# Kernel tuning notes

Hardware: AMD Instinct MI355X
Metric: run time of the kernel (lower is better)

Reference implementation:

```python
import jax, jax.numpy as jnp
import numpy as np

D_HEAD = 128


def setup_inputs() -> dict:
    key = jax.random.key(0)
    k1, k2, k3 = jax.random.split(key, 3)
    batch, num_q, seq_len, d = 16, 64, 4096, D_HEAD
    query = jax.random.normal(k1, (batch, num_q, d), dtype=jnp.float32)
    keys = jax.random.normal(k2, (batch, seq_len, d), dtype=jnp.float32)
    values = jax.random.normal(k3, (batch, seq_len, d), dtype=jnp.float32)
    return {"query": query, "keys": keys, "values": values}


def reference(query, keys, values):
    # AttentionJacobian.forward with 3D query -> compute_attention_jacobian_batched
    # J[b,q] = scale * ( sum_n a[b,q,n] v[b,n] k[b,n]^T  -  (a V)[b,q] ((a K)[b,q])^T )
    d_k = keys.shape[-1]
    scale = d_k ** (-0.5)
    scores = jnp.einsum('bqd,bnd->bqn', query, keys) * scale
    attn_weights = jax.nn.softmax(scores, axis=-1)            # (b, q, n)
    attn_outputs = jnp.einsum('bqn,bnv->bqv', attn_weights, values)
    # term1 without materializing (b, q, n, v, k): fuse as single contraction
    term1 = jnp.einsum('bqn,bnv,bnk->bqvk', attn_weights, values, keys)
    weighted_keys_sum = jnp.einsum('bqn,bnk->bqk', attn_weights, keys)
    term2 = jnp.einsum('bqv,bqk->bqvk', attn_outputs, weighted_keys_sum)
    jacobians = scale * (term1 - term2)                       # (b, q, d_v, d_k)
    return jacobians
```

## Files before the change

### kernel.cpp

```cpp
#include <hip/hip_runtime.h>
#include <stdint.h>

typedef _Float16 f16;
typedef _Float16 half8 __attribute__((ext_vector_type(8)));
typedef float f32x4 __attribute__((ext_vector_type(4)));

#define BATCH 16
#define NQ 64
#define SL 4096
#define DH 128


typedef __attribute__((address_space(3))) uint8_t lds8_t;
typedef __attribute__((address_space(1))) uint8_t glb8_t;

__device__ __forceinline__ void gload16(const void* g, void* l) {
  __builtin_amdgcn_global_load_lds((const glb8_t*)g, (lds8_t*)l, 16, 0, 0);
}

__global__ __launch_bounds__(256) void kprep(const float* __restrict__ Kg,
                                             const float* __restrict__ Vg,
                                             f16* __restrict__ Kt,
                                             f16* __restrict__ Vt) {
  __shared__ f16 Ld[128][130];
  const int blk = blockIdx.x;
  const int b = blk >> 6;
  const int tensor = (blk >> 5) & 1;
  const int chunk = blk & 31;
  const float* src = tensor ? Vg : Kg;
  f16* dst = tensor ? Vt : Kt;
  const int t = threadIdx.x;
  const int n0 = chunk * 128;
  {
    const int d = t & 127;
    const int nl = t >> 7;
    const float* s = src + ((size_t)b * SL + n0 + nl) * DH + d;
    for (int it = 0; it < 64; ++it)
      Ld[d][nl + it * 2] = (f16)s[(size_t)it * 2 * DH];
  }
  __syncthreads();
  {
    const int r = t & 15;
    const int kc = (t >> 4) & 3;
    const int w = t >> 6;
    char* dstb = (char*)(dst + (size_t)b * DH * SL);
#pragma unroll
    for (int tl = 0; tl < 4; ++tl)
#pragma unroll
      for (int hh = 0; hh < 2; ++hh) {
        const int dhi = w + hh * 4;
        const int d = dhi * 16 + r;
        const int nl = tl * 32 + kc * 8;
        const half8 v = *(const half8*)&Ld[d][nl];
        *(half8*)(dstb + (size_t)(chunk * 4 + tl) * 8192 + dhi * 1024 +
                  kc * 256 + r * 16) = v;
      }
  }
}

__global__ __launch_bounds__(256) void kscore(const float* __restrict__ Q,
                                              const f16* __restrict__ Kt,
                                              f16* __restrict__ E) {
  const int blk = (blockIdx.x & 7) * 64 + (blockIdx.x >> 3);
  __shared__ float Qs[8][128];
  const int b = blk >> 5;
  const int qg = (blk >> 2) & 7;
  const int ns = blk & 3;
  const int t = threadIdx.x;
  for (int i = t; i < 8 * 128; i += 256)
    Qs[i >> 7][i & 127] = Q[((size_t)b * NQ + qg * 8 + (i >> 7)) * DH + (i & 127)];
  __syncthreads();
  const int w = t >> 6, l = t & 63;
  const int q0 = (w >> 1) * 4;
  const int nbase = ns * 1024 + (w & 1) * 512 + l * 8;
  const f16* kb = Kt + (size_t)b * DH * SL + (size_t)(nbase >> 5) * 4096 +
                  (size_t)((nbase >> 3) & 3) * 128;
  float acc[4][8] = {};
  for (int d = 0; d < DH; ++d) {
    const half8 kv = *(const half8*)(kb + (d >> 4) * 512 + (d & 15) * 8);
    float kf[8];
#pragma unroll
    for (int j = 0; j < 8; ++j) kf[j] = (float)kv[j];
#pragma unroll
    for (int qi = 0; qi < 4; ++qi) {
      const float qv = Qs[q0 + qi][d];
#pragma unroll
      for (int j = 0; j < 8; ++j) acc[qi][j] += qv * kf[j];
    }
  }
  const float scl = 0.08838834764831845f;
#pragma unroll
  for (int qi = 0; qi < 4; ++qi) {
    half8 ev;
#pragma unroll
    for (int j = 0; j < 8; ++j) ev[j] = (f16)__expf(acc[qi][j] * scl);
    *(half8*)&E[((size_t)b * NQ + qg * 8 + q0 + qi) * SL + nbase] = ev;
  }
}

__global__ __launch_bounds__(256) void kreduce(const f16* __restrict__ E,
                                               float* __restrict__ denom) {
  const int gw = blockIdx.x * 4 + (threadIdx.x >> 6);
  const int lane = threadIdx.x & 63;
  const f16* e = E + (size_t)gw * SL;
  float s = 0.f;
#pragma unroll
  for (int i = 0; i < 8; ++i) {
    const half8 h = *(const half8*)(e + i * 512 + lane * 8);
#pragma unroll
    for (int j = 0; j < 8; ++j) s += (float)h[j];
  }
  for (int off = 1; off < 64; off <<= 1) s += __shfl_xor(s, off);
  if (lane == 0) denom[gw] = s;
}

__global__ __launch_bounds__(256) void kev(const f16* __restrict__ Vt,
                                           const f16* __restrict__ Kt,
                                           const f16* __restrict__ E,
                                           float* __restrict__ EVp,
                                           float* __restrict__ EKp) {
  const int blk = (blockIdx.x & 7) * 32 + (blockIdx.x >> 3);
  const int b = blk >> 4;
  const int tensor = (blk >> 3) & 1;
  const int qq = (blk >> 1) & 3;
  const int nh = blk & 1;
  const char* src = (const char*)((tensor ? Kt : Vt) + (size_t)b * DH * SL);
  float* dst = (tensor ? EKp : EVp) +
               ((size_t)nh * BATCH * NQ + (size_t)b * NQ + qq * 16) * DH;
  const f16* Eb = E + ((size_t)b * NQ + qq * 16) * SL;
  const int t = threadIdx.x, w = t >> 6, l = t & 63;
  f32x4 acc[2] = {};
  for (int n0 = nh * 2048; n0 < nh * 2048 + 2048; n0 += 32) {
    const half8 a0 =
        *(const half8*)(src + (size_t)(n0 >> 5) * 8192 + w * 1024 + l * 16);
    const half8 a1 =
        *(const half8*)(src + (size_t)(n0 >> 5) * 8192 + (w + 4) * 1024 + l * 16);
    const half8 b0 =
        *(const half8*)(Eb + (size_t)(l & 15) * SL + n0 + (l >> 4) * 8);
    acc[0] = __builtin_amdgcn_mfma_f32_16x16x32_f16(a0, b0, acc[0], 0, 0, 0);
    acc[1] = __builtin_amdgcn_mfma_f32_16x16x32_f16(a1, b0, acc[1], 0, 0, 0);
  }
#pragma unroll
  for (int sv2 = 0; sv2 < 2; ++sv2) {
    const int q = l & 15;
    const int row = (w + sv2 * 4) * 16 + (l >> 4) * 4;
    *(f32x4*)&dst[(size_t)q * DH + row] = acc[sv2];
  }
}

__global__ __launch_bounds__(256, 2) void kjac(
    const f16* __restrict__ Vt, const f16* __restrict__ Kt,
    const f16* __restrict__ E, const float* __restrict__ EV,
    const float* __restrict__ EK, const float* __restrict__ denom,
    float* __restrict__ out) {
  __shared__ __align__(16) f16 Vl[4][4096];
  __shared__ __align__(16) f16 Kl[4][4096];

  const int blk = (blockIdx.x & 7) * 64 + (blockIdx.x >> 3);
  const int b = blk >> 5;
  const int q0 = (blk & 31) * 2;
  const int t = threadIdx.x, w = t >> 6, l = t & 63;
  const int sA = (w >> 1) * 4;
  const int sB = (w & 1) * 4;
  const char* vtb = (const char*)(Vt + (size_t)b * DH * SL);
  const char* ktb = (const char*)(Kt + (size_t)b * DH * SL);
  const f16* Eb = E + ((size_t)b * NQ + q0) * SL;

  f32x4 acc[2][4][4] = {};
  half8 eA[2], eB[2];

#define STAGE(tile)                                                          \
  {                                                                          \
    const int bf = (tile) & 3;                                               \
    const size_t gb = (size_t)(tile) * 8192 + t * 16;                        \
    gload16(vtb + gb, (char*)Vl[bf] + t * 16);                               \
    gload16(vtb + gb + 4096, (char*)Vl[bf] + t * 16 + 4096);                 \
    gload16(ktb + gb, (char*)Kl[bf] + t * 16);                               \
    gload16(ktb + gb + 4096, (char*)Kl[bf] + t * 16 + 4096);                 \
  }

#define ELOAD(dst, tile)                                                     \
  {                                                                          \
    const int nn = (tile) * 32 + (l >> 4) * 8;                               \
    dst[0] = *(const half8*)(Eb + nn);                                       \
    dst[1] = *(const half8*)(Eb + SL + nn);                                  \
  }

#define COMPUTE(tile, e)                                                     \
  {                                                                          \
    const f16* vbuf = Vl[(tile) & 3];                                        \
    const f16* kbuf = Kl[(tile) & 3];                                        \
    half8 vf[4], kf[4];                                                      \
    _Pragma("unroll") for (int i = 0; i < 4; ++i) vf[i] =                    \
        *(const half8*)(vbuf + (sA + i) * 512 + l * 8);                      \
    _Pragma("unroll") for (int j = 0; j < 4; ++j) kf[j] =                    \
        *(const half8*)(kbuf + (sB + j) * 512 + l * 8);                      \
    __builtin_amdgcn_s_setprio(1);                                           \
    _Pragma("unroll") for (int i = 0; i < 4; ++i) {                          \
      const half8 u0 = e[0] * vf[i];                                         \
      const half8 u1 = e[1] * vf[i];                                         \
      _Pragma("unroll") for (int j = 0; j < 4; ++j) {                        \
        acc[0][i][j] = __builtin_amdgcn_mfma_f32_16x16x32_f16(               \
            u0, kf[j], acc[0][i][j], 0, 0, 0);                               \
        acc[1][i][j] = __builtin_amdgcn_mfma_f32_16x16x32_f16(               \
            u1, kf[j], acc[1][i][j], 0, 0, 0);                               \
      }                                                                      \
    }                                                                        \
    __builtin_amdgcn_s_setprio(0);                                           \
  }

#define BODY(tc, eu, el, wn)                                                 \
  {                                                                          \
    ELOAD(el, (tc) + 1)                                                      \
    STAGE((tc) + 2)                                                          \
    asm volatile("s_waitcnt vmcnt(" #wn ")" ::: "memory");                   \
    __builtin_amdgcn_s_barrier();                                            \
    COMPUTE((tc), eu)                                                        \
    __builtin_amdgcn_s_barrier();                                            \
  }

  ELOAD(eA, 0)
  STAGE(0)
  STAGE(1)
  BODY(0, eA, eB, 10)
  BODY(1, eB, eA, 12)
  BODY(2, eA, eB, 12)
  BODY(3, eB, eA, 12)
  for (int tt = 4; tt < 124; tt += 4) {
    BODY(tt + 0, eA, eB, 12)
    BODY(tt + 1, eB, eA, 12)
    BODY(tt + 2, eA, eB, 12)
    BODY(tt + 3, eB, eA, 12)
  }
  BODY(124, eA, eB, 12)
  BODY(125, eB, eA, 12)
  ELOAD(eB, 127)
  asm volatile("s_waitcnt vmcnt(8)" ::: "memory");
  __builtin_amdgcn_s_barrier();
  COMPUTE(126, eA)
  __builtin_amdgcn_s_barrier();
  asm volatile("s_waitcnt vmcnt(2)" ::: "memory");
  __builtin_amdgcn_s_barrier();
  COMPUTE(127, eB)
#undef STAGE
#undef ELOAD
#undef COMPUTE
#undef BODY

  const float scl = 0.08838834764831845f;
#pragma unroll
  for (int q = 0; q < 2; ++q) {
    const float invd = 1.0f / denom[b * NQ + q0 + q];
    const float* evq = EV + ((size_t)b * NQ + q0 + q) * DH;
    const float* evq2 = evq + (size_t)BATCH * NQ * DH;
    const float* ekq = EK + ((size_t)b * NQ + q0 + q) * DH;
    const float* ekq2 = ekq + (size_t)BATCH * NQ * DH;
    float* ob = out + (size_t)(b * NQ + q0 + q) * DH * DH;
#pragma unroll
    for (int i = 0; i < 4; ++i) {
      const int row0 = (sA + i) * 16 + (l >> 4) * 4;
      const f32x4 ev4 = *(const f32x4*)&evq[row0] + *(const f32x4*)&evq2[row0];
#pragma unroll
      for (int j = 0; j < 4; ++j) {
        const int col = (sB + j) * 16 + (l & 15);
        const float ek = ekq[col] + ekq2[col];
#pragma unroll
        for (int r = 0; r < 4; ++r)
          ob[(size_t)(row0 + r) * DH + col] =
              scl * invd * (acc[q][i][j][r] - invd * ev4[r] * ek);
      }
    }
  }
}

extern "C" void kernel_launch(void* const* d_in, const int* in_sizes, int n_in,
                              void* d_out, int out_size, void* d_ws,
                              size_t ws_size, hipStream_t stream) {
  const float* Q = (const float*)d_in[0];
  const float* K = (const float*)d_in[1];
  const float* V = (const float*)d_in[2];
  float* out = (float*)d_out;

  f16* Vt = (f16*)d_ws;
  f16* Kt = Vt + (size_t)BATCH * DH * SL;
  f16* Ef = Kt + (size_t)BATCH * DH * SL;
  float* EV = (float*)(Ef + (size_t)BATCH * NQ * SL);
  float* EK = EV + 2 * (size_t)BATCH * NQ * DH;
  float* denom = EK + 2 * (size_t)BATCH * NQ * DH;

  kprep<<<1024, 256, 0, stream>>>(K, V, Kt, Vt);
  kscore<<<512, 256, 0, stream>>>(Q, Kt, Ef);
  kreduce<<<256, 256, 0, stream>>>(Ef, denom);
  kev<<<256, 256, 0, stream>>>(Vt, Kt, Ef, EV, EK);
  kjac<<<512, 256, 0, stream>>>(Vt, Kt, Ef, EV, EK, denom, out);
}
```

Before: 193.8 us.

## Use 512-thread kjac blocks with register double-buffered fragments and single barrier

Doubles the kjac block to 8 waves, each owning a 64x32 output slice, so per-wave accumulators shrink and more waves hide latency. The main loop is restructured: the next tile's LDS fragments and E vectors are preloaded into alternating register sets, staging runs three tiles ahead, and each phase uses one barrier instead of two. Each thread now issues one global-to-LDS load per matrix per tile. The risks are higher register pressure from the double-buffered fragments and possible LDS read conflicts, since 8 waves per block at 2 blocks per CU must fit the register file.

Result: slower. 237.8 us (+22.7%).

```diff
diff --git a/kernel.cpp b/kernel.cpp
--- a/kernel.cpp
+++ b/kernel.cpp
@@ -148,7 +148,7 @@
   }
 }
 
-__global__ __launch_bounds__(256, 2) void kjac(
+__global__ __launch_bounds__(512, 2) void kjac(
     const f16* __restrict__ Vt, const f16* __restrict__ Kt,
     const f16* __restrict__ E, const float* __restrict__ EV,
     const float* __restrict__ EK, const float* __restrict__ denom,
@@ -160,46 +160,47 @@
   const int b = blk >> 5;
   const int q0 = (blk & 31) * 2;
   const int t = threadIdx.x, w = t >> 6, l = t & 63;
-  const int sA = (w >> 1) * 4;
-  const int sB = (w & 1) * 4;
+  const int rh = w >> 2;
+  const int cq = w & 3;
   const char* vtb = (const char*)(Vt + (size_t)b * DH * SL);
   const char* ktb = (const char*)(Kt + (size_t)b * DH * SL);
   const f16* Eb = E + ((size_t)b * NQ + q0) * SL;
 
-  f32x4 acc[2][4][4] = {};
-  half8 eA[2], eB[2];
+  f32x4 acc[2][4][2] = {};
+  half8 vfA[4], kfA[2], vfB[4], kfB[2], eA[2], eB[2];
 
 #define STAGE(tile)                                                          \
   {                                                                          \
-    const int bf = (tile) & 3;                                               \
     const size_t gb = (size_t)(tile) * 8192 + t * 16;                        \
-    gload16(vtb + gb, (char*)Vl[bf] + t * 16);                               \
-    gload16(vtb + gb + 4096, (char*)Vl[bf] + t * 16 + 4096);                 \
-    gload16(ktb + gb, (char*)Kl[bf] + t * 16);                               \
-    gload16(ktb + gb + 4096, (char*)Kl[bf] + t * 16 + 4096);                 \
-  }
-
-#define ELOAD(dst, tile)                                                     \
+    const int bi = (tile) & 3;                                               \
+    gload16(vtb + gb, (char*)Vl[bi] + t * 16);                               \
+    gload16(ktb + gb, (char*)Kl[bi] + t * 16);                               \
+  }
+
+#define ELOAD(e, tile)                                                       \
   {                                                                          \
     const int nn = (tile) * 32 + (l >> 4) * 8;                               \
-    dst[0] = *(const half8*)(Eb + nn);                                       \
-    dst[1] = *(const half8*)(Eb + SL + nn);                                  \
-  }
-
-#define COMPUTE(tile, e)                                                     \
+    e[0] = *(const half8*)(Eb + nn);                                         \
+    e[1] = *(const half8*)(Eb + SL + nn);                                    \
+  }
+
+#define FLOAD(vf, kf, tile)                                                  \
   {                                                                          \
     const f16* vbuf = Vl[(tile) & 3];                                        \
     const f16* kbuf = Kl[(tile) & 3];                                        \
-    half8 vf[4], kf[4];                                                      \
     _Pragma("unroll") for (int i = 0; i < 4; ++i) vf[i] =                    \
-        *(const half8*)(vbuf + (sA + i) * 512 + l * 8);                      \
-    _Pragma("unroll") for (int j = 0; j < 4; ++j) kf[j] =                    \
-        *(const half8*)(kbuf + (sB + j) * 512 + l * 8);                      \
+        *(const half8*)(vbuf + (rh * 4 + i) * 512 + l * 8);                  \
+    _Pragma("unroll") for (int j = 0; j < 2; ++j) kf[j] =                    \
+        *(const half8*)(kbuf + (cq * 2 + j) * 512 + l * 8);                  \
+  }
+
+#define MFMA8(vf, kf, e)                                                     \
+  {                                                                          \
     __builtin_amdgcn_s_setprio(1);                                           \
     _Pragma("unroll") for (int i = 0; i < 4; ++i) {                          \
       const half8 u0 = e[0] * vf[i];                                         \
       const half8 u1 = e[1] * vf[i];                                         \
-      _Pragma("unroll") for (int j = 0; j < 4; ++j) {                        \
+      _Pragma("unroll") for (int j = 0; j < 2; ++j) {                        \
         acc[0][i][j] = __builtin_amdgcn_mfma_f32_16x16x32_f16(               \
             u0, kf[j], acc[0][i][j], 0, 0, 0);                               \
         acc[1][i][j] = __builtin_amdgcn_mfma_f32_16x16x32_f16(               \
@@ -209,43 +210,32 @@
     __builtin_amdgcn_s_setprio(0);                                           \
   }
 
-#define BODY(tc, eu, el, wn)                                                 \
-  {                                                                          \
-    ELOAD(el, (tc) + 1)                                                      \
-    STAGE((tc) + 2)                                                          \
-    asm volatile("s_waitcnt vmcnt(" #wn ")" ::: "memory");                   \
-    __builtin_amdgcn_s_barrier();                                            \
-    COMPUTE((tc), eu)                                                        \
-    __builtin_amdgcn_s_barrier();                                            \
+#define PHASE(TC, CVF, CKF, CE, NVF, NKF, NE, VM, DOST)                      \
+  {                                                                          \
+    asm volatile("s_waitcnt vmcnt(" #VM ")\n\ts_barrier" ::: "memory");      \
+    ELOAD(NE, (TC) + 1)                                                      \
+    FLOAD(NVF, NKF, (TC) + 1)                                                \
+    if (DOST) STAGE((TC) + 3)                                                \
+    MFMA8(CVF, CKF, CE)                                                      \
   }
 
   ELOAD(eA, 0)
-  STAGE(0)
-  STAGE(1)
-  BODY(0, eA, eB, 10)
-  BODY(1, eB, eA, 12)
-  BODY(2, eA, eB, 12)
-  BODY(3, eB, eA, 12)
-  for (int tt = 4; tt < 124; tt += 4) {
-    BODY(tt + 0, eA, eB, 12)
-    BODY(tt + 1, eB, eA, 12)
-    BODY(tt + 2, eA, eB, 12)
-    BODY(tt + 3, eB, eA, 12)
-  }
-  BODY(124, eA, eB, 12)
-  BODY(125, eB, eA, 12)
-  ELOAD(eB, 127)
-  asm volatile("s_waitcnt vmcnt(8)" ::: "memory");
-  __builtin_amdgcn_s_barrier();
-  COMPUTE(126, eA)
-  __builtin_amdgcn_s_barrier();
-  asm volatile("s_waitcnt vmcnt(2)" ::: "memory");
-  __builtin_amdgcn_s_barrier();
-  COMPUTE(127, eB)
+  STAGE(0) STAGE(1) STAGE(2)
+  asm volatile("s_waitcnt vmcnt(4)\n\ts_barrier" ::: "memory");
+  FLOAD(vfA, kfA, 0)
+  PHASE(0, vfA, kfA, eA, vfB, kfB, eB, 2, 1)
+  for (int tt = 1; tt < 125; tt += 2) {
+    PHASE(tt, vfB, kfB, eB, vfA, kfA, eA, 4, 1)
+    PHASE(tt + 1, vfA, kfA, eA, vfB, kfB, eB, 4, 1)
+  }
+  PHASE(125, vfB, kfB, eB, vfA, kfA, eA, 4, 0)
+  PHASE(126, vfA, kfA, eA, vfB, kfB, eB, 2, 0)
+  MFMA8(vfB, kfB, eB)
 #undef STAGE
 #undef ELOAD
-#undef COMPUTE
-#undef BODY
+#undef FLOAD
+#undef MFMA8
+#undef PHASE
 
   const float scl = 0.08838834764831845f;
 #pragma unroll
@@ -258,11 +248,11 @@
     float* ob = out + (size_t)(b * NQ + q0 + q) * DH * DH;
 #pragma unroll
     for (int i = 0; i < 4; ++i) {
-      const int row0 = (sA + i) * 16 + (l >> 4) * 4;
+      const int row0 = rh * 64 + i * 16 + (l >> 4) * 4;
       const f32x4 ev4 = *(const f32x4*)&evq[row0] + *(const f32x4*)&evq2[row0];
 #pragma unroll
-      for (int j = 0; j < 4; ++j) {
-        const int col = (sB + j) * 16 + (l & 15);
+      for (int j = 0; j < 2; ++j) {
+        const int col = cq * 32 + j * 16 + (l & 15);
         const float ek = ekq[col] + ekq2[col];
 #pragma unroll
         for (int r = 0; r < 4; ++r)
@@ -292,5 +282,5 @@
   kscore<<<512, 256, 0, stream>>>(Q, Kt, Ef);
   kreduce<<<256, 256, 0, stream>>>(Ef, denom);
   kev<<<256, 256, 0, stream>>>(Vt, Kt, Ef, EV, EK);
-  kjac<<<512, 256, 0, stream>>>(Vt, Kt, Ef, EV, EK, denom, out);
-}
+  kjac<<<512, 512, 0, stream>>>(Vt, Kt, Ef, EV, EK, denom, out);
+}
```

## Load V/K fragments directly from global into registers, dropping LDS staging

Applied to the files above, without the earlier changes.

Replaces the four-deep LDS ring buffer (global_load_lds plus barriers) in the Jacobian kernel with direct per-wave global loads of V, K and E fragments into registers, double-buffered across tiles. This removes the LDS traffic and the two workgroup barriers per tile. In exchange, waves that share V or K rows now fetch them separately from global/L2, which raises cache traffic, and register pressure rises with two fragment sets live at once. Latency hiding now relies only on the register prefetch distance of one tile.

New measurement: 185.9 us. -4.1%, faster.

```diff
diff --git a/kernel.cpp b/kernel.cpp
--- a/kernel.cpp
+++ b/kernel.cpp
@@ -10,13 +10,6 @@
 #define SL 4096
 #define DH 128
 
-
-typedef __attribute__((address_space(3))) uint8_t lds8_t;
-typedef __attribute__((address_space(1))) uint8_t glb8_t;
-
-__device__ __forceinline__ void gload16(const void* g, void* l) {
-  __builtin_amdgcn_global_load_lds((const glb8_t*)g, (lds8_t*)l, 16, 0, 0);
-}
 
 __global__ __launch_bounds__(256) void kprep(const float* __restrict__ Kg,
                                              const float* __restrict__ Vg,
@@ -153,52 +146,36 @@
     const f16* __restrict__ E, const float* __restrict__ EV,
     const float* __restrict__ EK, const float* __restrict__ denom,
     float* __restrict__ out) {
-  __shared__ __align__(16) f16 Vl[4][4096];
-  __shared__ __align__(16) f16 Kl[4][4096];
-
   const int blk = (blockIdx.x & 7) * 64 + (blockIdx.x >> 3);
   const int b = blk >> 5;
   const int q0 = (blk & 31) * 2;
   const int t = threadIdx.x, w = t >> 6, l = t & 63;
   const int sA = (w >> 1) * 4;
   const int sB = (w & 1) * 4;
-  const char* vtb = (const char*)(Vt + (size_t)b * DH * SL);
-  const char* ktb = (const char*)(Kt + (size_t)b * DH * SL);
-  const f16* Eb = E + ((size_t)b * NQ + q0) * SL;
+  const char* vtb = (const char*)(Vt + (size_t)b * DH * SL) + sA * 1024 + l * 16;
+  const char* ktb = (const char*)(Kt + (size_t)b * DH * SL) + sB * 1024 + l * 16;
+  const f16* Eb = E + ((size_t)b * NQ + q0) * SL + (l >> 4) * 8;
 
   f32x4 acc[2][4][4] = {};
-  half8 eA[2], eB[2];
-
-#define STAGE(tile)                                                          \
+  half8 vfA[4], kfA[4], efA[2], vfB[4], kfB[4], efB[2];
+
+#define LOADF(vf, kf, ef, tile)                                              \
   {                                                                          \
-    const int bf = (tile) & 3;                                               \
-    const size_t gb = (size_t)(tile) * 8192 + t * 16;                        \
-    gload16(vtb + gb, (char*)Vl[bf] + t * 16);                               \
-    gload16(vtb + gb + 4096, (char*)Vl[bf] + t * 16 + 4096);                 \
-    gload16(ktb + gb, (char*)Kl[bf] + t * 16);                               \
-    gload16(ktb + gb + 4096, (char*)Kl[bf] + t * 16 + 4096);                 \
-  }
-
-#define ELOAD(dst, tile)                                                     \
+    const size_t gb = (size_t)(tile) * 8192;                                 \
+    _Pragma("unroll") for (int i = 0; i < 4; ++i) vf[i] =                    \
+        *(const half8*)(vtb + gb + i * 1024);                                \
+    _Pragma("unroll") for (int j = 0; j < 4; ++j) kf[j] =                    \
+        *(const half8*)(ktb + gb + j * 1024);                                \
+    ef[0] = *(const half8*)(Eb + (tile) * 32);                               \
+    ef[1] = *(const half8*)(Eb + SL + (tile) * 32);                          \
+  }
+
+#define MFMA32(vf, kf, ef)                                                   \
   {                                                                          \
-    const int nn = (tile) * 32 + (l >> 4) * 8;                               \
-    dst[0] = *(const half8*)(Eb + nn);                                       \
-    dst[1] = *(const half8*)(Eb + SL + nn);                                  \
-  }
-
-#define COMPUTE(tile, e)                                                     \
-  {                                                                          \
-    const f16* vbuf = Vl[(tile) & 3];                                        \
-    const f16* kbuf = Kl[(tile) & 3];                                        \
-    half8 vf[4], kf[4];                                                      \
-    _Pragma("unroll") for (int i = 0; i < 4; ++i) vf[i] =                    \
-        *(const half8*)(vbuf + (sA + i) * 512 + l * 8);                      \
-    _Pragma("unroll") for (int j = 0; j < 4; ++j) kf[j] =                    \
-        *(const half8*)(kbuf + (sB + j) * 512 + l * 8);                      \
     __builtin_amdgcn_s_setprio(1);                                           \
     _Pragma("unroll") for (int i = 0; i < 4; ++i) {                          \
-      const half8 u0 = e[0] * vf[i];                                         \
-      const half8 u1 = e[1] * vf[i];                                         \
+      const half8 u0 = ef[0] * vf[i];                                        \
+      const half8 u1 = ef[1] * vf[i];                                        \
       _Pragma("unroll") for (int j = 0; j < 4; ++j) {                        \
         acc[0][i][j] = __builtin_amdgcn_mfma_f32_16x16x32_f16(               \
             u0, kf[j], acc[0][i][j], 0, 0, 0);                               \
@@ -209,43 +186,18 @@
     __builtin_amdgcn_s_setprio(0);                                           \
   }
 
-#define BODY(tc, eu, el, wn)                                                 \
-  {                                                                          \
-    ELOAD(el, (tc) + 1)                                                      \
-    STAGE((tc) + 2)                                                          \
-    asm volatile("s_waitcnt vmcnt(" #wn ")" ::: "memory");                   \
-    __builtin_amdgcn_s_barrier();                                            \
-    COMPUTE((tc), eu)                                                        \
-    __builtin_amdgcn_s_barrier();                                            \
-  }
-
-  ELOAD(eA, 0)
-  STAGE(0)
-  STAGE(1)
-  BODY(0, eA, eB, 10)
-  BODY(1, eB, eA, 12)
-  BODY(2, eA, eB, 12)
-  BODY(3, eB, eA, 12)
-  for (int tt = 4; tt < 124; tt += 4) {
-    BODY(tt + 0, eA, eB, 12)
-    BODY(tt + 1, eB, eA, 12)
-    BODY(tt + 2, eA, eB, 12)
-    BODY(tt + 3, eB, eA, 12)
-  }
-  BODY(124, eA, eB, 12)
-  BODY(125, eB, eA, 12)
-  ELOAD(eB, 127)
-  asm volatile("s_waitcnt vmcnt(8)" ::: "memory");
-  __builtin_amdgcn_s_barrier();
-  COMPUTE(126, eA)
-  __builtin_amdgcn_s_barrier();
-  asm volatile("s_waitcnt vmcnt(2)" ::: "memory");
-  __builtin_amdgcn_s_barrier();
-  COMPUTE(127, eB)
-#undef STAGE
-#undef ELOAD
-#undef COMPUTE
-#undef BODY
+  LOADF(vfA, kfA, efA, 0)
+  for (int tt = 0; tt < 126; tt += 2) {
+    LOADF(vfB, kfB, efB, tt + 1)
+    MFMA32(vfA, kfA, efA)
+    LOADF(vfA, kfA, efA, tt + 2)
+    MFMA32(vfB, kfB, efB)
+  }
+  LOADF(vfB, kfB, efB, 127)
+  MFMA32(vfA, kfA, efA)
+  MFMA32(vfB, kfB, efB)
+#undef LOADF
+#undef MFMA32
 
   const float scl = 0.08838834764831845f;
 #pragma unroll
```
